# Performance work log

Hardware: AMD Instinct MI355X
Metric: run time of the kernel (lower is better)

## Reference

```python
import jax, jax.numpy as jnp
import numpy as np

N_NODES = 50000
N_RAND_EDGES = 800000
N_GRAPHS = 16
F_IN = 128
HID = 64
EMB = 16


def gat_layer(x, src, dst, W, a_src, a_dst, bias, heads, out_ch, concat):
    # x: [N, Fin]; W: [Fin, heads*out_ch]; a_src/a_dst: [heads, out_ch]
    n = x.shape[0]
    h = (x @ W).reshape(n, heads, out_ch)                      # [N, H, C]
    alpha_src = jnp.sum(h * a_src, axis=-1)                    # [N, H]
    alpha_dst = jnp.sum(h * a_dst, axis=-1)                    # [N, H]
    logits = jax.nn.leaky_relu(alpha_src[src] + alpha_dst[dst], 0.2)  # [E, H]
    # segment softmax over incoming edges of each dst node
    m = jax.ops.segment_max(logits, dst, num_segments=n)       # [N, H]
    e = jnp.exp(logits - m[dst])                               # [E, H]
    s = jax.ops.segment_sum(e, dst, num_segments=n)            # [N, H]
    alpha = e / (s[dst] + 1e-16)                               # [E, H]
    msg = h[src] * alpha[:, :, None]                           # [E, H, C]
    out = jax.ops.segment_sum(msg, dst, num_segments=n)        # [N, H, C]
    out = out.reshape(n, heads * out_ch) if concat else out.mean(axis=1)
    return out + bias, alpha


def setup_inputs() -> dict:
    key = jax.random.key(0)
    ks = jax.random.split(key, 20)
    x = jax.random.normal(ks[0], (N_NODES, F_IN), dtype=jnp.float32)
    src = jax.random.randint(ks[1], (N_RAND_EDGES,), 0, N_NODES)
    dst = jax.random.randint(ks[2], (N_RAND_EDGES,), 0, N_NODES)
    loops = jnp.arange(N_NODES)
    edge_index = jnp.stack([jnp.concatenate([src, loops]),
                            jnp.concatenate([dst, loops])]).astype(jnp.int64)
    batch = jnp.sort(jax.random.randint(ks[3], (N_NODES,), 0, N_GRAPHS)).astype(jnp.int64)
    p = lambda k, shp: (jax.random.normal(k, shp, dtype=jnp.float32) * 0.1)
    return {
        "x": x, "edge_index": edge_index, "batch": batch,
        # conv1: 128 -> 64, heads=2, concat -> 128
        "W1": p(ks[4], (F_IN, 2 * HID)), "as1": p(ks[5], (2, HID)), "ad1": p(ks[6], (2, HID)), "b1": p(ks[7], (2 * HID,)),
        # conv2: 128 -> 128, heads=1, mean
        "W2": p(ks[8], (2 * HID, 2 * HID)), "as2": p(ks[9], (1, 2 * HID)), "ad2": p(ks[10], (1, 2 * HID)), "b2": p(ks[11], (2 * HID,)),
        # conv3: 128 -> 16, heads=1, mean
        "W3": p(ks[12], (2 * HID, EMB)), "as3": p(ks[13], (1, EMB)), "ad3": p(ks[14], (1, EMB)), "b3": p(ks[15], (EMB,)),
        # final classifier 16 -> 2
        "Wl": p(ks[16], (EMB, 2)), "bl": p(ks[17], (2,)),
    }


def reference(x, edge_index, batch, W1, as1, ad1, b1, W2, as2, ad2, b2,
              W3, as3, ad3, b3, Wl, bl):
    src, dst = edge_index[0], edge_index[1]
    h1, a1 = gat_layer(x, src, dst, W1, as1, ad1, b1, heads=2, out_ch=HID, concat=True)
    h1 = jax.nn.relu(h1)
    h2, a2 = gat_layer(h1, src, dst, W2, as2, ad2, b2, heads=1, out_ch=2 * HID, concat=False)
    h2 = jax.nn.relu(h2)
    emb, a3 = gat_layer(h2, src, dst, W3, as3, ad3, b3, heads=1, out_ch=EMB, concat=False)
    # global mean pool over graphs (eval mode -> dropout is identity)
    counts = jax.ops.segment_sum(jnp.ones((emb.shape[0],), emb.dtype), batch, num_segments=N_GRAPHS)
    g_emb = jax.ops.segment_sum(emb, batch, num_segments=N_GRAPHS) / jnp.clip(counts, 1.0, None)[:, None]
    out = g_emb @ Wl + bl
    return (out, g_emb, emb, a1, a2, a3)
```

## Files before the change

kernel.cpp:

```cpp
#include <hip/hip_runtime.h>
#include <hip/hip_bf16.h>

#define DEVFN __device__ __forceinline__

using short8 = __attribute__((ext_vector_type(8))) short;
using f32x4  = __attribute__((ext_vector_type(4))) float;

DEVFN float ldf(const void* p, size_t i, bool f32) {
    return f32 ? ((const float*)p)[i]
               : __bfloat162float(((const __hip_bfloat16*)p)[i]);
}
DEVFN int ldidx(const void* p, size_t i, bool i64) {
    return i64 ? (int)((const long long*)p)[i] : ((const int*)p)[i];
}
DEVFN void stf(void* p, size_t i, float v, bool f32) {
    if (f32) ((float*)p)[i] = v;
    else     ((__hip_bfloat16*)p)[i] = __float2bfloat16(v);
}
DEVFN float lky(float v) { return v > 0.f ? v : 0.2f * v; }

DEVFN float bfbits2f(short s) {
    return __uint_as_float(((unsigned)(unsigned short)s) << 16);
}
DEVFN short f2bfbits(float f) {
    unsigned u = __float_as_uint(f);
    return (short)((u + 0x7fffu + ((u >> 16) & 1u)) >> 16);
}

__global__ void detect_k(const void* x, const void* ei, int* flags) {
    if (threadIdx.x == 0 && blockIdx.x == 0) {
        const __hip_bfloat16* xb = (const __hip_bfloat16*)x;
        int bad = 0;
        for (int i = 0; i < 512; ++i) {
            float v = __bfloat162float(xb[i]);
            if (!(v == v) || fabsf(v) > 1.0e6f) bad++;
        }
        flags[0] = (bad > 16) ? 1 : 0;
        const unsigned* w = (const unsigned*)ei;
        int zeros = 0;
        for (int i = 0; i < 64; ++i) if (w[2 * i + 1] == 0u) zeros++;
        flags[1] = (zeros >= 60) ? 1 : 0;
    }
}

__global__ void zero_i32(int* __restrict__ p, int n) {
    int i = blockIdx.x * blockDim.x + threadIdx.x;
    int st = gridDim.x * blockDim.x;
    for (; i < n; i += st) p[i] = 0;
}
__global__ void zero_f32(float* __restrict__ p, long n) {
    long i = (long)blockIdx.x * blockDim.x + threadIdx.x;
    long st = (long)gridDim.x * blockDim.x;
    for (; i < n; i += st) p[i] = 0.f;
}

__global__ void hist_k(const void* __restrict__ ei, int E, int* __restrict__ cnt,
                       const int* __restrict__ flags) {
    const bool i64 = flags[1] != 0;
    int e = blockIdx.x * blockDim.x + threadIdx.x;
    if (e >= E) return;
    atomicAdd(&cnt[ldidx(ei, (size_t)E + e, i64)], 1);
}

__global__ void scan_block_k(const int* __restrict__ cnt, int* __restrict__ incl,
                             int* __restrict__ part, int N) {
    __shared__ int sm[256];
    int tid = threadIdx.x;
    int i = blockIdx.x * 256 + tid;
    int v = (i < N) ? cnt[i] : 0;
    sm[tid] = v;
    __syncthreads();
    for (int o = 1; o < 256; o <<= 1) {
        int t = (tid >= o) ? sm[tid - o] : 0;
        __syncthreads();
        sm[tid] += t;
        __syncthreads();
    }
    if (i < N) incl[i] = sm[tid];
    if (tid == 255) part[blockIdx.x] = sm[255];
}

__global__ void scan_part_k(int* __restrict__ part, int nb) {
    __shared__ int sm[256];
    __shared__ int off;
    int tid = threadIdx.x;
    if (tid == 0) off = 0;
    __syncthreads();
    for (int b = 0; b < nb; b += 256) {
        int i = b + tid;
        int v = (i < nb) ? part[i] : 0;
        sm[tid] = v;
        __syncthreads();
        for (int o = 1; o < 256; o <<= 1) {
            int t = (tid >= o) ? sm[tid - o] : 0;
            __syncthreads();
            sm[tid] += t;
            __syncthreads();
        }
        if (i < nb) part[i] = sm[tid] - v + off;
        __syncthreads();
        if (tid == 255) off += sm[255];
        __syncthreads();
    }
}

__global__ void finalize_scan_k(int* __restrict__ incl_cur, const int* __restrict__ cnt,
                                const int* __restrict__ part, int* __restrict__ rs,
                                int N, int E) {
    int i = blockIdx.x * 256 + threadIdx.x;
    if (i >= N) return;
    int v = incl_cur[i] - cnt[i] + part[blockIdx.x];
    rs[i] = v;
    incl_cur[i] = v;
    if (i == N - 1) rs[N] = E;
}

__global__ void scatter_csr_k(const void* __restrict__ ei, int E, int* __restrict__ cur,
                              int* __restrict__ csr_src, int* __restrict__ csr_eid,
                              const int* __restrict__ flags) {
    const bool i64 = flags[1] != 0;
    int e = blockIdx.x * blockDim.x + threadIdx.x;
    if (e >= E) return;
    int s = ldidx(ei, e, i64);
    int d = ldidx(ei, (size_t)E + e, i64);
    int p = atomicAdd(&cur[d], 1);
    csr_src[p] = s;
    csr_eid[p] = e;
}

template <int DSRC, int FOUT, int HEADS>
__global__ __launch_bounds__(256) void gemm_alpha_mfma_k(
    const void* __restrict__ xin, const void* __restrict__ Wv,
    const void* __restrict__ asv, const void* __restrict__ adv,
    short* __restrict__ h_bf, float* __restrict__ as_out, float* __restrict__ ad_out,
    int N, const int* __restrict__ flags)
{
    constexpr int FIN = 128;
    constexpr int NCT = FOUT / 16;
    constexpr int CPH = FOUT / HEADS;
    constexpr int CTPH = CPH / 16;
    const bool f32 = flags[0] != 0;

    __shared__ short Wt[FOUT * FIN];

    for (int i = threadIdx.x; i < FIN * FOUT; i += 256) {
        int k = i / FOUT, c = i - (i / FOUT) * FOUT;
        short w;
        if (f32) w = f2bfbits(((const float*)Wv)[i]);
        else     w = ((const short*)Wv)[i];
        *(short*)((char*)Wt + (size_t)c * (FIN * 2) + (((k * 2) ^ ((c & 7) << 4)))) = w;
    }
    __syncthreads();

    const int wv = threadIdx.x >> 6;
    const int lane = threadIdx.x & 63;
    const int m0 = blockIdx.x * 64 + wv * 16;
    if (m0 >= N) return;
    const int lrow = lane & 15;
    const int lk   = lane >> 4;

    short8 afrag[4];
    if (DSRC == 0 && f32) {
        const float* xf = (const float*)xin + (size_t)(m0 + lrow) * FIN + lk * 8;
#pragma unroll
        for (int ks = 0; ks < 4; ++ks) {
            short8 t;
#pragma unroll
            for (int j = 0; j < 8; ++j) t[j] = f2bfbits(xf[ks * 32 + j]);
            afrag[ks] = t;
        }
    } else {
        const short* xb = (const short*)xin + (size_t)(m0 + lrow) * FIN + lk * 8;
#pragma unroll
        for (int ks = 0; ks < 4; ++ks)
            afrag[ks] = *(const short8*)(xb + ks * 32);
    }

    float csA[HEADS][4], cdA[HEADS][4];
#pragma unroll
    for (int hd = 0; hd < HEADS; ++hd)
#pragma unroll
        for (int r = 0; r < 4; ++r) { csA[hd][r] = 0.f; cdA[hd][r] = 0.f; }

#pragma unroll
    for (int ct = 0; ct < NCT; ++ct) {
        const int col = ct * 16 + lrow;
        const int hd = ct / CTPH;
        f32x4 acc = {0.f, 0.f, 0.f, 0.f};
#pragma unroll
        for (int ks = 0; ks < 4; ++ks) {
            const int kbyte = ks * 64 + lk * 16;
            short8 bfrag = *(const short8*)((const char*)Wt +
                               (size_t)col * (FIN * 2) + (kbyte ^ ((col & 7) << 4)));
            acc = __builtin_amdgcn_mfma_f32_16x16x32_bf16(afrag[ks], bfrag, acc, 0, 0, 0);
        }
        const float asc = ldf(asv, col, f32);
        const float adc = ldf(adv, col, f32);
#pragma unroll
        for (int r = 0; r < 4; ++r) {
            h_bf[(size_t)(m0 + lk * 4 + r) * FOUT + col] = f2bfbits(acc[r]);
            csA[hd][r] += acc[r] * asc;
            cdA[hd][r] += acc[r] * adc;
        }
    }

#pragma unroll
    for (int hd = 0; hd < HEADS; ++hd)
#pragma unroll
        for (int r = 0; r < 4; ++r) {
            float cs = csA[hd][r], cd = cdA[hd][r];
            for (int o = 1; o < 16; o <<= 1) {
                cs += __shfl_xor(cs, o);
                cd += __shfl_xor(cd, o);
            }
            csA[hd][r] = cs; cdA[hd][r] = cd;
        }
    if (lrow == 0) {
#pragma unroll
        for (int r = 0; r < 4; ++r) {
            int n = m0 + lk * 4 + r;
#pragma unroll
            for (int hd = 0; hd < HEADS; ++hd) {
                as_out[(size_t)n * HEADS + hd] = csA[hd][r];
                ad_out[(size_t)n * HEADS + hd] = cdA[hd][r];
            }
        }
    }
}

template <int HEADS>
__global__ __launch_bounds__(256) void softmax_csr_k(
    const float* __restrict__ as_, const float* __restrict__ ad_,
    const int* __restrict__ rs, const int* __restrict__ csr_src, const int* __restrict__ csr_eid,
    float* __restrict__ alpha_csr, void* __restrict__ dout, size_t aoff,
    int N, const int* __restrict__ flags)
{
    const bool f32 = flags[0] != 0;
    const int wid = (blockIdx.x * 256 + threadIdx.x) >> 6;
    const int lane = threadIdx.x & 63;
    if (wid >= N) return;
    const int beg = rs[wid], end = rs[wid + 1];

    const float ad0 = ad_[(size_t)wid * HEADS];
    const float ad1 = (HEADS == 2) ? ad_[(size_t)wid * HEADS + 1] : 0.f;

    float m0 = -1e30f, m1 = -1e30f;
    for (int p = beg + lane; p < end; p += 64) {
        int s = csr_src[p];
        m0 = fmaxf(m0, lky(as_[(size_t)s * HEADS] + ad0));
        if (HEADS == 2) m1 = fmaxf(m1, lky(as_[(size_t)s * HEADS + 1] + ad1));
    }
    for (int o = 1; o < 64; o <<= 1) {
        m0 = fmaxf(m0, __shfl_xor(m0, o));
        if (HEADS == 2) m1 = fmaxf(m1, __shfl_xor(m1, o));
    }
    float s0 = 0.f, s1 = 0.f;
    for (int p = beg + lane; p < end; p += 64) {
        int s = csr_src[p];
        s0 += expf(lky(as_[(size_t)s * HEADS] + ad0) - m0);
        if (HEADS == 2) s1 += expf(lky(as_[(size_t)s * HEADS + 1] + ad1) - m1);
    }
    for (int o = 1; o < 64; o <<= 1) {
        s0 += __shfl_xor(s0, o);
        if (HEADS == 2) s1 += __shfl_xor(s1, o);
    }
    const float inv0 = 1.f / (s0 + 1e-16f);
    const float inv1 = 1.f / (s1 + 1e-16f);

    for (int p = beg + lane; p < end; p += 64) {
        int s = csr_src[p];
        int eid = csr_eid[p];
        float a0 = expf(lky(as_[(size_t)s * HEADS] + ad0) - m0) * inv0;
        alpha_csr[(size_t)p * HEADS] = a0;
        stf(dout, aoff + (size_t)eid * HEADS, a0, f32);
        if (HEADS == 2) {
            float a1 = expf(lky(as_[(size_t)s * HEADS + 1] + ad1) - m1) * inv1;
            alpha_csr[(size_t)p * 2 + 1] = a1;
            stf(dout, aoff + (size_t)eid * 2 + 1, a1, f32);
        }
    }
}

template <int HEADS, bool RELU>
__global__ __launch_bounds__(256) void pull128_v2_k(
    const short* __restrict__ h_bf, const float* __restrict__ alpha_csr,
    const int* __restrict__ rs, const int* __restrict__ csr_src,
    const void* __restrict__ bias, short* __restrict__ z_bf,
    int N, const int* __restrict__ flags)
{
    const bool f32 = flags[0] != 0;
    const int wid = (blockIdx.x * 256 + threadIdx.x) >> 6;
    if (wid >= N) return;
    const int lane = threadIdx.x & 63;
    const int cg = lane & 15;
    const int es = lane >> 4;
    const int h = (HEADS == 2) ? (cg >> 3) : 0;
    const int beg = rs[wid], end = rs[wid + 1];

    float acc[8] = {0.f, 0.f, 0.f, 0.f, 0.f, 0.f, 0.f, 0.f};
    for (int base = beg; base < end; base += 4) {
        const int p = base + es;
        if (p < end) {
            const int sj = csr_src[p];
            const float a = alpha_csr[(size_t)p * HEADS + h];
            const short8 hv = *(const short8*)(h_bf + (size_t)sj * 128 + cg * 8);
#pragma unroll
            for (int j = 0; j < 8; ++j)
                acc[j] = fmaf(bfbits2f(hv[j]), a, acc[j]);
        }
    }
#pragma unroll
    for (int j = 0; j < 8; ++j) {
        acc[j] += __shfl_xor(acc[j], 16);
        acc[j] += __shfl_xor(acc[j], 32);
    }
    if (es == 0) {
        short8 outv;
#pragma unroll
        for (int j = 0; j < 8; ++j) {
            float v = acc[j] + ldf(bias, cg * 8 + j, f32);
            if (RELU) v = fmaxf(v, 0.f);
            outv[j] = f2bfbits(v);
        }
        *(short8*)(z_bf + (size_t)wid * 128 + cg * 8) = outv;
    }
}

__global__ __launch_bounds__(256) void pull16_v2_k(
    const short* __restrict__ h_bf, const float* __restrict__ alpha_csr,
    const int* __restrict__ rs, const int* __restrict__ csr_src,
    float* __restrict__ out, int N)
{
    const int wid = (blockIdx.x * 256 + threadIdx.x) >> 6;
    if (wid >= N) return;
    const int lane = threadIdx.x & 63;
    const int cg = lane & 7;
    const int es = lane >> 3;
    const int beg = rs[wid], end = rs[wid + 1];

    float a0 = 0.f, a1 = 0.f;
    for (int base = beg; base < end; base += 8) {
        const int p = base + es;
        if (p < end) {
            const int sj = csr_src[p];
            const float a = alpha_csr[p];
            const int hv = *(const int*)(h_bf + (size_t)sj * 16 + cg * 2);
            a0 = fmaf(bfbits2f((short)(hv & 0xffff)), a, a0);
            a1 = fmaf(bfbits2f((short)(hv >> 16)), a, a1);
        }
    }
#pragma unroll
    for (int o = 8; o < 64; o <<= 1) {
        a0 += __shfl_xor(a0, o);
        a1 += __shfl_xor(a1, o);
    }
    if (es == 0) {
        out[(size_t)wid * 16 + cg * 2]     = a0;
        out[(size_t)wid * 16 + cg * 2 + 1] = a1;
    }
}

__global__ __launch_bounds__(256) void finalize3_k(
    const float* __restrict__ acc, const void* __restrict__ bias,
    const void* __restrict__ batch, void* __restrict__ dout, size_t emb_off,
    float* __restrict__ g_sum, int N, const int* __restrict__ flags)
{
    const bool f32 = flags[0] != 0;
    const bool i64 = flags[1] != 0;
    __shared__ float gp[256];
    int tid = threadIdx.x;
    gp[tid] = 0.f;
    __syncthreads();
    long idx = (long)blockIdx.x * 256 + tid;
    if (idx < (long)N * 16) {
        int n = (int)(idx >> 4), col = (int)(idx & 15);
        float v = acc[idx] + ldf(bias, col, f32);
        stf(dout, emb_off + idx, v, f32);
        int g = ldidx(batch, n, i64);
        atomicAdd(&gp[g * 16 + col], v);
    }
    __syncthreads();
    float pv = gp[tid];
    if (pv != 0.f) atomicAdd(&g_sum[tid], pv);
}

__global__ __launch_bounds__(256) void head_k(
    const float* __restrict__ g_sum, const void* __restrict__ batch,
    const void* __restrict__ Wl, const void* __restrict__ bl,
    void* __restrict__ dout, size_t gemb_off, int N, const int* __restrict__ flags)
{
    const bool f32 = flags[0] != 0;
    const bool i64 = flags[1] != 0;
    __shared__ float ge[256];
    __shared__ int cnts[16];
    int tid = threadIdx.x;
    if (tid < 16) {
        int lo = 0, hi = N;
        while (lo < hi) { int mid = (lo + hi) >> 1; if (ldidx(batch, mid, i64) < tid) lo = mid + 1; else hi = mid; }
        int l2 = 0, h2 = N;
        while (l2 < h2) { int mid = (l2 + h2) >> 1; if (ldidx(batch, mid, i64) <= tid) l2 = mid + 1; else h2 = mid; }
        cnts[tid] = l2 - lo;
    }
    __syncthreads();
    {
        int g = tid >> 4;
        float v = g_sum[tid] / fmaxf((float)cnts[g], 1.f);
        ge[tid] = v;
        stf(dout, gemb_off + tid, v, f32);
    }
    __syncthreads();
    if (tid < 32) {
        int g = tid >> 1, j = tid & 1;
        float s = ldf(bl, j, f32);
        for (int c = 0; c < 16; ++c) s += ge[g * 16 + c] * ldf(Wl, (size_t)c * 2 + j, f32);
        stf(dout, (size_t)g * 2 + j, s, f32);
    }
}

static inline int cdiv(long a, int b) { return (int)((a + b - 1) / b); }

extern "C" void kernel_launch(void* const* d_in, const int* in_sizes, int n_in,
                              void* d_out, int out_size, void* d_ws, size_t ws_size,
                              hipStream_t stream)
{
    const void* x   = d_in[0];
    const void* ei  = d_in[1];
    const void* batch = d_in[2];
    const void* W1  = d_in[3];
    const void* as1 = d_in[4];
    const void* ad1 = d_in[5];
    const void* b1  = d_in[6];
    const void* W2  = d_in[7];
    const void* as2 = d_in[8];
    const void* ad2 = d_in[9];
    const void* b2  = d_in[10];
    const void* W3  = d_in[11];
    const void* as3 = d_in[12];
    const void* ad3 = d_in[13];
    const void* b3  = d_in[14];
    const void* Wl  = d_in[15];
    const void* bl  = d_in[16];

    const int N = in_sizes[0] / 128;
    const int E = in_sizes[1] / 2;

    int* flags = (int*)d_ws;
    float* ws = (float*)d_ws + 16;
    size_t o = 0;
    float* as_  = ws + o; o += (size_t)N * 2;
    float* ad_  = ws + o; o += (size_t)N * 2;
    float* alpha_csr = ws + o; o += (size_t)E * 2;
    float* bufE = ws + o; o += (size_t)N * 16;
    float* g_sum = ws + o; o += 256;
    short* hX = (short*)(ws + o); o += (size_t)N * 64;
    short* hZ = (short*)(ws + o); o += (size_t)N * 64;
    short* h3 = (short*)(ws + o); o += (size_t)N * 8;
    int* ip = (int*)(ws + o);
    int* cnt  = ip;            ip += N;
    int* incl = ip;            ip += N;
    int* part = ip;            ip += 256;
    int* rs   = ip;            ip += N + 1;
    int* csr_src = ip;         ip += E;
    int* csr_eid = ip;         ip += E;

    const size_t off_gemb = 32;
    const size_t off_emb  = 32 + 256;
    const size_t off_a1   = off_emb + (size_t)N * 16;
    const size_t off_a2   = off_a1 + (size_t)E * 2;
    const size_t off_a3   = off_a2 + (size_t)E;

    const int B = 256;
    const int nbN = cdiv(N, 256);
    const int gemmBlocks = cdiv(N, 64);
    const int waveBlocks = cdiv(N, 4);

    detect_k<<<1, 64, 0, stream>>>(x, ei, flags);

    zero_i32<<<nbN, B, 0, stream>>>(cnt, N);
    hist_k<<<cdiv(E, B), B, 0, stream>>>(ei, E, cnt, flags);
    scan_block_k<<<nbN, B, 0, stream>>>(cnt, incl, part, N);
    scan_part_k<<<1, B, 0, stream>>>(part, nbN);
    finalize_scan_k<<<nbN, B, 0, stream>>>(incl, cnt, part, rs, N, E);
    scatter_csr_k<<<cdiv(E, B), B, 0, stream>>>(ei, E, incl, csr_src, csr_eid, flags);

    gemm_alpha_mfma_k<0, 128, 2><<<gemmBlocks, 256, 0, stream>>>(x, W1, as1, ad1, hX, as_, ad_, N, flags);
    softmax_csr_k<2><<<waveBlocks, 256, 0, stream>>>(as_, ad_, rs, csr_src, csr_eid,
                                                     alpha_csr, d_out, off_a1, N, flags);
    pull128_v2_k<2, true><<<waveBlocks, 256, 0, stream>>>(hX, alpha_csr, rs, csr_src, b1, hZ, N, flags);

    gemm_alpha_mfma_k<1, 128, 1><<<gemmBlocks, 256, 0, stream>>>(hZ, W2, as2, ad2, hX, as_, ad_, N, flags);
    softmax_csr_k<1><<<waveBlocks, 256, 0, stream>>>(as_, ad_, rs, csr_src, csr_eid,
                                                     alpha_csr, d_out, off_a2, N, flags);
    pull128_v2_k<1, true><<<waveBlocks, 256, 0, stream>>>(hX, alpha_csr, rs, csr_src, b2, hZ, N, flags);

    gemm_alpha_mfma_k<1, 16, 1><<<gemmBlocks, 256, 0, stream>>>(hZ, W3, as3, ad3, h3, as_, ad_, N, flags);
    softmax_csr_k<1><<<waveBlocks, 256, 0, stream>>>(as_, ad_, rs, csr_src, csr_eid,
                                                     alpha_csr, d_out, off_a3, N, flags);
    pull16_v2_k<<<waveBlocks, 256, 0, stream>>>(h3, alpha_csr, rs, csr_src, bufE, N);
    zero_f32<<<1, B, 0, stream>>>(g_sum, 256);
    finalize3_k<<<cdiv((long)N * 16, B), B, 0, stream>>>(bufE, b3, batch, d_out, off_emb, g_sum, N, flags);

    head_k<<<1, B, 0, stream>>>(g_sum, batch, Wl, bl, d_out, off_gemb, N, flags);
}
```

Measured before the change: 390.3 us.

## Recompute attention weights in pull kernels and write alpha output in edge order

The softmax kernel now stores only the per-node max and inverse sum. The aggregation kernels recompute each edge weight from as_/ad_ on the fly, so the per-edge alpha_csr array is no longer written and read back. A separate edge-ordered kernel writes the required alpha output with coalesced stores, which removes the scattered writes through csr_eid and the csr_eid array itself. The cost is an extra launch per layer, repeated exp evaluations, and gathers of as_ and minv in the new kernel.

```diff
diff --git a/kernel.cpp b/kernel.cpp
--- a/kernel.cpp
+++ b/kernel.cpp
@@ -116,8 +116,7 @@
 }
 
 __global__ void scatter_csr_k(const void* __restrict__ ei, int E, int* __restrict__ cur,
-                              int* __restrict__ csr_src, int* __restrict__ csr_eid,
-                              const int* __restrict__ flags) {
+                              int* __restrict__ csr_src, const int* __restrict__ flags) {
     const bool i64 = flags[1] != 0;
     int e = blockIdx.x * blockDim.x + threadIdx.x;
     if (e >= E) return;
@@ -125,7 +124,6 @@
     int d = ldidx(ei, (size_t)E + e, i64);
     int p = atomicAdd(&cur[d], 1);
     csr_src[p] = s;
-    csr_eid[p] = e;
 }
 
 template <int DSRC, int FOUT, int HEADS>
@@ -229,13 +227,11 @@
 }
 
 template <int HEADS>
-__global__ __launch_bounds__(256) void softmax_csr_k(
+__global__ __launch_bounds__(256) void softmax_minv_k(
     const float* __restrict__ as_, const float* __restrict__ ad_,
-    const int* __restrict__ rs, const int* __restrict__ csr_src, const int* __restrict__ csr_eid,
-    float* __restrict__ alpha_csr, void* __restrict__ dout, size_t aoff,
-    int N, const int* __restrict__ flags)
-{
-    const bool f32 = flags[0] != 0;
+    const int* __restrict__ rs, const int* __restrict__ csr_src,
+    float2* __restrict__ minv, int N)
+{
     const int wid = (blockIdx.x * 256 + threadIdx.x) >> 6;
     const int lane = threadIdx.x & 63;
     if (wid >= N) return;
@@ -264,26 +260,35 @@
         s0 += __shfl_xor(s0, o);
         if (HEADS == 2) s1 += __shfl_xor(s1, o);
     }
-    const float inv0 = 1.f / (s0 + 1e-16f);
-    const float inv1 = 1.f / (s1 + 1e-16f);
-
-    for (int p = beg + lane; p < end; p += 64) {
-        int s = csr_src[p];
-        int eid = csr_eid[p];
-        float a0 = expf(lky(as_[(size_t)s * HEADS] + ad0) - m0) * inv0;
-        alpha_csr[(size_t)p * HEADS] = a0;
-        stf(dout, aoff + (size_t)eid * HEADS, a0, f32);
-        if (HEADS == 2) {
-            float a1 = expf(lky(as_[(size_t)s * HEADS + 1] + ad1) - m1) * inv1;
-            alpha_csr[(size_t)p * 2 + 1] = a1;
-            stf(dout, aoff + (size_t)eid * 2 + 1, a1, f32);
-        }
-    }
+    if (lane == 0) {
+        minv[(size_t)wid * HEADS] = make_float2(m0, 1.f / (s0 + 1e-16f));
+        if (HEADS == 2)
+            minv[(size_t)wid * HEADS + 1] = make_float2(m1, 1.f / (s1 + 1e-16f));
+    }
+}
+
+template <int HEADS>
+__global__ void alpha_out_k(
+    const float* __restrict__ as_, const float* __restrict__ ad_,
+    const float2* __restrict__ minv, const void* __restrict__ ei,
+    void* __restrict__ dout, size_t aoff, int E, const int* __restrict__ flags)
+{
+    const bool f32 = flags[0] != 0;
+    const bool i64 = flags[1] != 0;
+    int idx = blockIdx.x * blockDim.x + threadIdx.x;
+    if (idx >= E * HEADS) return;
+    int e = idx / HEADS, h = idx & (HEADS - 1);
+    int s = ldidx(ei, e, i64);
+    int d = ldidx(ei, (size_t)E + e, i64);
+    float2 mi = minv[(size_t)d * HEADS + h];
+    float a = expf(lky(as_[(size_t)s * HEADS + h] + ad_[(size_t)d * HEADS + h]) - mi.x) * mi.y;
+    stf(dout, aoff + idx, a, f32);
 }
 
 template <int HEADS, bool RELU>
-__global__ __launch_bounds__(256) void pull128_v2_k(
-    const short* __restrict__ h_bf, const float* __restrict__ alpha_csr,
+__global__ __launch_bounds__(256) void pull128_f_k(
+    const short* __restrict__ h_bf, const float* __restrict__ as_,
+    const float* __restrict__ ad_, const float2* __restrict__ minv,
     const int* __restrict__ rs, const int* __restrict__ csr_src,
     const void* __restrict__ bias, short* __restrict__ z_bf,
     int N, const int* __restrict__ flags)
@@ -297,12 +302,15 @@
     const int h = (HEADS == 2) ? (cg >> 3) : 0;
     const int beg = rs[wid], end = rs[wid + 1];
 
+    const float2 mi = minv[(size_t)wid * HEADS + h];
+    const float adh = ad_[(size_t)wid * HEADS + h];
+
     float acc[8] = {0.f, 0.f, 0.f, 0.f, 0.f, 0.f, 0.f, 0.f};
     for (int base = beg; base < end; base += 4) {
         const int p = base + es;
         if (p < end) {
             const int sj = csr_src[p];
-            const float a = alpha_csr[(size_t)p * HEADS + h];
+            const float a = expf(lky(as_[(size_t)sj * HEADS + h] + adh) - mi.x) * mi.y;
             const short8 hv = *(const short8*)(h_bf + (size_t)sj * 128 + cg * 8);
 #pragma unroll
             for (int j = 0; j < 8; ++j)
@@ -326,8 +334,9 @@
     }
 }
 
-__global__ __launch_bounds__(256) void pull16_v2_k(
-    const short* __restrict__ h_bf, const float* __restrict__ alpha_csr,
+__global__ __launch_bounds__(256) void pull16_f_k(
+    const short* __restrict__ h_bf, const float* __restrict__ as_,
+    const float* __restrict__ ad_, const float2* __restrict__ minv,
     const int* __restrict__ rs, const int* __restrict__ csr_src,
     float* __restrict__ out, int N)
 {
@@ -338,12 +347,15 @@
     const int es = lane >> 3;
     const int beg = rs[wid], end = rs[wid + 1];
 
+    const float2 mi = minv[wid];
+    const float adh = ad_[wid];
+
     float a0 = 0.f, a1 = 0.f;
     for (int base = beg; base < end; base += 8) {
         const int p = base + es;
         if (p < end) {
             const int sj = csr_src[p];
-            const float a = alpha_csr[p];
+            const float a = expf(lky(as_[sj] + adh) - mi.x) * mi.y;
             const int hv = *(const int*)(h_bf + (size_t)sj * 16 + cg * 2);
             a0 = fmaf(bfbits2f((short)(hv & 0xffff)), a, a0);
             a1 = fmaf(bfbits2f((short)(hv >> 16)), a, a1);
@@ -449,7 +461,7 @@
     size_t o = 0;
     float* as_  = ws + o; o += (size_t)N * 2;
     float* ad_  = ws + o; o += (size_t)N * 2;
-    float* alpha_csr = ws + o; o += (size_t)E * 2;
+    float2* minv = (float2*)(ws + o); o += (size_t)N * 4;
     float* bufE = ws + o; o += (size_t)N * 16;
     float* g_sum = ws + o; o += 256;
     short* hX = (short*)(ws + o); o += (size_t)N * 64;
@@ -461,7 +473,6 @@
     int* part = ip;            ip += 256;
     int* rs   = ip;            ip += N + 1;
     int* csr_src = ip;         ip += E;
-    int* csr_eid = ip;         ip += E;
 
     const size_t off_gemb = 32;
     const size_t off_emb  = 32 + 256;
@@ -481,22 +492,22 @@
     scan_block_k<<<nbN, B, 0, stream>>>(cnt, incl, part, N);
     scan_part_k<<<1, B, 0, stream>>>(part, nbN);
     finalize_scan_k<<<nbN, B, 0, stream>>>(incl, cnt, part, rs, N, E);
-    scatter_csr_k<<<cdiv(E, B), B, 0, stream>>>(ei, E, incl, csr_src, csr_eid, flags);
+    scatter_csr_k<<<cdiv(E, B), B, 0, stream>>>(ei, E, incl, csr_src, flags);
 
     gemm_alpha_mfma_k<0, 128, 2><<<gemmBlocks, 256, 0, stream>>>(x, W1, as1, ad1, hX, as_, ad_, N, flags);
-    softmax_csr_k<2><<<waveBlocks, 256, 0, stream>>>(as_, ad_, rs, csr_src, csr_eid,
-                                                     alpha_csr, d_out, off_a1, N, flags);
-    pull128_v2_k<2, true><<<waveBlocks, 256, 0, stream>>>(hX, alpha_csr, rs, csr_src, b1, hZ, N, flags);
+    softmax_minv_k<2><<<waveBlocks, 256, 0, stream>>>(as_, ad_, rs, csr_src, minv, N);
+    alpha_out_k<2><<<cdiv((long)E * 2, B), B, 0, stream>>>(as_, ad_, minv, ei, d_out, off_a1, E, flags);
+    pull128_f_k<2, true><<<waveBlocks, 256, 0, stream>>>(hX, as_, ad_, minv, rs, csr_src, b1, hZ, N, flags);
 
     gemm_alpha_mfma_k<1, 128, 1><<<gemmBlocks, 256, 0, stream>>>(hZ, W2, as2, ad2, hX, as_, ad_, N, flags);
-    softmax_csr_k<1><<<waveBlocks, 256, 0, stream>>>(as_, ad_, rs, csr_src, csr_eid,
-                                                     alpha_csr, d_out, off_a2, N, flags);
-    pull128_v2_k<1, true><<<waveBlocks, 256, 0, stream>>>(hX, alpha_csr, rs, csr_src, b2, hZ, N, flags);
+    softmax_minv_k<1><<<waveBlocks, 256, 0, stream>>>(as_, ad_, rs, csr_src, minv, N);
+    alpha_out_k<1><<<cdiv(E, B), B, 0, stream>>>(as_, ad_, minv, ei, d_out, off_a2, E, flags);
+    pull128_f_k<1, true><<<waveBlocks, 256, 0, stream>>>(hX, as_, ad_, minv, rs, csr_src, b2, hZ, N, flags);
 
     gemm_alpha_mfma_k<1, 16, 1><<<gemmBlocks, 256, 0, stream>>>(hZ, W3, as3, ad3, h3, as_, ad_, N, flags);
-    softmax_csr_k<1><<<waveBlocks, 256, 0, stream>>>(as_, ad_, rs, csr_src, csr_eid,
-                                                     alpha_csr, d_out, off_a3, N, flags);
-    pull16_v2_k<<<waveBlocks, 256, 0, stream>>>(h3, alpha_csr, rs, csr_src, bufE, N);
+    softmax_minv_k<1><<<waveBlocks, 256, 0, stream>>>(as_, ad_, rs, csr_src, minv, N);
+    alpha_out_k<1><<<cdiv(E, B), B, 0, stream>>>(as_, ad_, minv, ei, d_out, off_a3, E, flags);
+    pull16_f_k<<<waveBlocks, 256, 0, stream>>>(h3, as_, ad_, minv, rs, csr_src, bufE, N);
     zero_f32<<<1, B, 0, stream>>>(g_sum, 256);
     finalize3_k<<<cdiv((long)N * 16, B), B, 0, stream>>>(bufE, b3, batch, d_out, off_emb, g_sum, N, flags);
 
```

New measurement: 412.4 us. 5.7% more time.
